# Kernel optimization log

Measured on AMD Instinct MI355X. Metric: run time of the kernel, lower is better.

## Reference

```python
import jax, jax.numpy as jnp
import numpy as np

B, C_IN, T = 8, 1024, 8192
K, D = 1024, 8  # codebook_size, codebook_dim


def setup_inputs() -> dict:
    key = jax.random.key(0)
    ks = jax.random.split(key, 6)
    z = jax.random.normal(ks[0], (B, C_IN, T), dtype=jnp.float32)
    # effective (post weight-norm) 1x1 conv weights, kernel dim squeezed
    in_w = jax.random.normal(ks[1], (D, C_IN), dtype=jnp.float32) * (1.0 / np.sqrt(C_IN))
    in_b = jax.random.normal(ks[2], (D,), dtype=jnp.float32) * 0.01
    codebook = jax.random.normal(ks[3], (K, D), dtype=jnp.float32)
    out_w = jax.random.normal(ks[4], (C_IN, D), dtype=jnp.float32) * (1.0 / np.sqrt(D))
    out_b = jax.random.normal(ks[5], (C_IN,), dtype=jnp.float32) * 0.01
    return {"z": z, "in_w": in_w, "in_b": in_b, "codebook": codebook,
            "out_w": out_w, "out_b": out_b}


def reference(z, in_w, in_b, codebook, out_w, out_b):
    # in_proj: 1x1 Conv1d over channels  [B,C,T] -> [B,D,T]
    z_e = jnp.einsum('bct,dc->bdt', z, in_w) + in_b[None, :, None]
    enc = z_e.transpose(0, 2, 1).reshape(-1, z_e.shape[1])  # [B*T, D]
    # squared-L2 distance to every codebook entry: ||e||^2 - 2 e.w + ||w||^2
    dist = ((enc * enc).sum(1, keepdims=True)
            - 2.0 * enc @ codebook.T
            + (codebook * codebook).sum(1)[None, :])  # [B*T, K]
    ids = jnp.argmax(-dist, axis=1).reshape(z.shape[0], -1)  # [B, T]
    # decode: embedding gather + 1x1 out_proj  [B,T,D] -> [B,C,T]
    z_q = codebook[ids]  # [B, T, D]
    out = jnp.einsum('btd,cd->bct', z_q, out_w) + out_b[None, :, None]
    return out, ids
```

## Files before the change

kernel.cpp:

```cpp
#include <hip/hip_runtime.h>

#define B_   8
#define C_   1024
#define T_   8192
#define K_   1024
#define D_   8
#define CT_  (C_ * T_)
#define BT_  (B_ * T_)
#define OUTN_ ((size_t)B_ * CT_)

__global__ __launch_bounds__(256) void vq_encode_kernel(
    const float* __restrict__ z, const float* __restrict__ in_w,
    const float* __restrict__ in_b, const float* __restrict__ cb,
    float* __restrict__ ids_f)
{
    __shared__ float s_inwT[C_ * D_];
    __shared__ float s_nrm[K_];
    __shared__ float s_encp[4][D_][64];
    __shared__ float s_val[4][64];
    __shared__ int   s_idx[4][64];

    const int tid = threadIdx.x;
    const int w   = tid >> 6;
    const int l   = tid & 63;
    const int bt0 = blockIdx.x * 64;
    const int b   = bt0 >> 13;
    const int t0  = bt0 & (T_ - 1);

    for (int i = tid; i < C_ * D_; i += 256) {
        const int d = i >> 10;
        const int c = i & (C_ - 1);
        s_inwT[c * D_ + d] = in_w[i];
    }
    {
        float ib[D_];
#pragma unroll
        for (int d = 0; d < D_; ++d) ib[d] = in_b[d];
#pragma unroll
        for (int j = 0; j < 4; ++j) {
            const int k = tid + j * 256;
            const float4* cp = (const float4*)(cb + k * D_);
            const float4 a = cp[0], q = cp[1];
            const float ss = a.x*a.x + a.y*a.y + a.z*a.z + a.w*a.w
                           + q.x*q.x + q.y*q.y + q.z*q.z + q.w*q.w;
            const float qq = ib[0]*a.x + ib[1]*a.y + ib[2]*a.z + ib[3]*a.w
                           + ib[4]*q.x + ib[5]*q.y + ib[6]*q.z + ib[7]*q.w;
            s_nrm[k] = 0.5f * ss - qq;
        }
    }
    __syncthreads();

    float acc[D_];
#pragma unroll
    for (int d = 0; d < D_; ++d) acc[d] = 0.0f;
    const float* zp = z + (size_t)b * CT_ + (size_t)(w * 256) * T_ + (t0 + l);
#pragma unroll 8
    for (int i = 0; i < 256; ++i) {
        const float zv = zp[(size_t)i * T_];
        const float4* wp = (const float4*)&s_inwT[(w * 256 + i) * D_];
        const float4 w0 = wp[0], w1 = wp[1];
        acc[0] = fmaf(zv, w0.x, acc[0]);
        acc[1] = fmaf(zv, w0.y, acc[1]);
        acc[2] = fmaf(zv, w0.z, acc[2]);
        acc[3] = fmaf(zv, w0.w, acc[3]);
        acc[4] = fmaf(zv, w1.x, acc[4]);
        acc[5] = fmaf(zv, w1.y, acc[5]);
        acc[6] = fmaf(zv, w1.z, acc[6]);
        acc[7] = fmaf(zv, w1.w, acc[7]);
    }
#pragma unroll
    for (int d = 0; d < D_; ++d) s_encp[w][d][l] = acc[d];
    __syncthreads();

    for (int p = tid; p < 512; p += 256) {
        const int d = p >> 6, tt = p & 63;
        s_encp[0][d][tt] = s_encp[0][d][tt] + s_encp[1][d][tt]
                         + s_encp[2][d][tt] + s_encp[3][d][tt];
    }
    __syncthreads();

    float e[D_];
#pragma unroll
    for (int d = 0; d < D_; ++d) e[d] = s_encp[0][d][l];

    const int wu = __builtin_amdgcn_readfirstlane(w);
    float best = 3.4e38f;
    int   bi   = 0;
    for (int j = 0; j < 256; ++j) {
        const int k = wu * 256 + j;
        const float4* cp = (const float4*)(cb + k * D_);
        const float4 a = cp[0], q = cp[1];
        float s = s_nrm[k];
        s = fmaf(-e[0], a.x, s);
        s = fmaf(-e[1], a.y, s);
        s = fmaf(-e[2], a.z, s);
        s = fmaf(-e[3], a.w, s);
        s = fmaf(-e[4], q.x, s);
        s = fmaf(-e[5], q.y, s);
        s = fmaf(-e[6], q.z, s);
        s = fmaf(-e[7], q.w, s);
        if (s < best) { best = s; bi = k; }
    }
    s_val[w][l] = best;
    s_idx[w][l] = bi;
    __syncthreads();

    if (tid < 64) {
        float bv = s_val[0][l];
        int   bb = s_idx[0][l];
#pragma unroll
        for (int ww = 1; ww < 4; ++ww) {
            const float v = s_val[ww][l];
            if (v < bv) { bv = v; bb = s_idx[ww][l]; }
        }
        ids_f[bt0 + l] = (float)bb;
    }
}

__global__ __launch_bounds__(256) void vq_decode_kernel(
    const float* __restrict__ ids_f, const float* __restrict__ cb,
    const float* __restrict__ out_w, const float* __restrict__ out_b,
    float* __restrict__ out)
{
    __shared__ float s_cbT[D_ * K_];

    const int tid = threadIdx.x;
    for (int i = tid; i < K_ * D_ / 4; i += 256) {
        const float4 v = ((const float4*)cb)[i];
        const int k = i >> 1;
        const int d0 = (i & 1) * 4;
        s_cbT[(d0 + 0) * K_ + k] = v.x;
        s_cbT[(d0 + 1) * K_ + k] = v.y;
        s_cbT[(d0 + 2) * K_ + k] = v.z;
        s_cbT[(d0 + 3) * K_ + k] = v.w;
    }
    __syncthreads();

    const int blk = blockIdx.x;
    const int bt0 = (blk >> 3) * 1024;
    const int c0  = (blk & 7) * 128;
    const int b   = bt0 >> 13;
    const int tt  = (bt0 & (T_ - 1)) + tid * 4;

    const float4 idv = *(const float4*)(ids_f + bt0 + tid * 4);
    const int k0 = (int)idv.x, k1 = (int)idv.y, k2 = (int)idv.z, k3 = (int)idv.w;

    float r0[D_], r1[D_], r2[D_], r3[D_];
#pragma unroll
    for (int d = 0; d < D_; ++d) {
        r0[d] = s_cbT[d * K_ + k0];
        r1[d] = s_cbT[d * K_ + k1];
        r2[d] = s_cbT[d * K_ + k2];
        r3[d] = s_cbT[d * K_ + k3];
    }

    float* op = out + (size_t)b * CT_ + (size_t)c0 * T_ + tt;
#pragma unroll 4
    for (int j = 0; j < 128; ++j) {
        const int c = c0 + j;
        const float4* wp = (const float4*)(out_w + c * D_);
        const float4 w0 = wp[0], w1 = wp[1];
        const float bias = out_b[c];
        float wr[D_];
        wr[0] = w0.x; wr[1] = w0.y; wr[2] = w0.z; wr[3] = w0.w;
        wr[4] = w1.x; wr[5] = w1.y; wr[6] = w1.z; wr[7] = w1.w;
        float4 o;
        o.x = bias; o.y = bias; o.z = bias; o.w = bias;
#pragma unroll
        for (int d = 0; d < D_; ++d) {
            o.x = fmaf(r0[d], wr[d], o.x);
            o.y = fmaf(r1[d], wr[d], o.y);
            o.z = fmaf(r2[d], wr[d], o.z);
            o.w = fmaf(r3[d], wr[d], o.w);
        }
        *(float4*)(op + (size_t)j * T_) = o;
    }
}

extern "C" void kernel_launch(void* const* d_in, const int* in_sizes, int n_in,
                              void* d_out, int out_size, void* d_ws, size_t ws_size,
                              hipStream_t stream) {
    const float* z    = (const float*)d_in[0];
    const float* in_w = (const float*)d_in[1];
    const float* in_b = (const float*)d_in[2];
    const float* cb   = (const float*)d_in[3];
    const float* ow   = (const float*)d_in[4];
    const float* ob   = (const float*)d_in[5];

    float* out   = (float*)d_out;
    float* ids_f = out + OUTN_;

    vq_encode_kernel<<<BT_ / 64, 256, 0, stream>>>(z, in_w, in_b, cb, ids_f);
    vq_decode_kernel<<<(BT_ / 1024) * 8, 256, 0, stream>>>(ids_f, cb, ow, ob, out);
}
```

Measured before the change: 554.7 us.

## Fuse encode and decode into one kernel with a separate prep kernel

Moves the transposed in_proj weights and the codebook norm/bias term into a small prep kernel that writes to workspace, so the main kernel no longer fills 36KB of LDS per block. Encode, argmin and decode now run in one kernel: each block decodes its own 64 timesteps using the chosen codebook rows staged in LDS, which removes the ids round trip and the second launch. The smaller LDS footprint and launch_bounds(256,4) are meant to raise occupancy. In exchange, weights are read from global/scalar memory instead of LDS, and output stores become scalar 64-wide rows instead of float4.

```diff
diff --git a/kernel.cpp b/kernel.cpp
--- a/kernel.cpp
+++ b/kernel.cpp
@@ -9,171 +9,117 @@
 #define BT_  (B_ * T_)
 #define OUTN_ ((size_t)B_ * CT_)
 
-__global__ __launch_bounds__(256) void vq_encode_kernel(
-    const float* __restrict__ z, const float* __restrict__ in_w,
-    const float* __restrict__ in_b, const float* __restrict__ cb,
-    float* __restrict__ ids_f)
+__global__ __launch_bounds__(256) void vq_prep(
+    const float* __restrict__ in_w, const float* __restrict__ in_b,
+    const float* __restrict__ cb, float* __restrict__ wT,
+    float* __restrict__ nrm)
 {
-    __shared__ float s_inwT[C_ * D_];
-    __shared__ float s_nrm[K_];
-    __shared__ float s_encp[4][D_][64];
-    __shared__ float s_val[4][64];
-    __shared__ int   s_idx[4][64];
+    const int i = blockIdx.x * 256 + threadIdx.x;
+    if (i < C_ * D_) {
+        const int d = i >> 10;
+        const int c = i & (C_ - 1);
+        wT[c * D_ + d] = in_w[i];
+    }
+    if (i < K_) {
+        float s = 0.0f, q = 0.0f;
+#pragma unroll
+        for (int d = 0; d < D_; ++d) {
+            const float w = cb[i * D_ + d];
+            s = fmaf(w, w, s);
+            q = fmaf(in_b[d], w, q);
+        }
+        nrm[i] = 0.5f * s - q;
+    }
+}
+
+__global__ __launch_bounds__(256, 4) void vq_fused(
+    const float* __restrict__ z, const float* __restrict__ wT,
+    const float* __restrict__ nrm, const float* __restrict__ cb,
+    const float* __restrict__ out_w, const float* __restrict__ out_b,
+    float* __restrict__ out, float* __restrict__ ids_f)
+{
+    __shared__ float s_p[2048];
 
     const int tid = threadIdx.x;
-    const int w   = tid >> 6;
+    const int wu  = __builtin_amdgcn_readfirstlane(tid >> 6);
     const int l   = tid & 63;
     const int bt0 = blockIdx.x * 64;
     const int b   = bt0 >> 13;
     const int t0  = bt0 & (T_ - 1);
-
-    for (int i = tid; i < C_ * D_; i += 256) {
-        const int d = i >> 10;
-        const int c = i & (C_ - 1);
-        s_inwT[c * D_ + d] = in_w[i];
-    }
-    {
-        float ib[D_];
-#pragma unroll
-        for (int d = 0; d < D_; ++d) ib[d] = in_b[d];
-#pragma unroll
-        for (int j = 0; j < 4; ++j) {
-            const int k = tid + j * 256;
-            const float4* cp = (const float4*)(cb + k * D_);
-            const float4 a = cp[0], q = cp[1];
-            const float ss = a.x*a.x + a.y*a.y + a.z*a.z + a.w*a.w
-                           + q.x*q.x + q.y*q.y + q.z*q.z + q.w*q.w;
-            const float qq = ib[0]*a.x + ib[1]*a.y + ib[2]*a.z + ib[3]*a.w
-                           + ib[4]*q.x + ib[5]*q.y + ib[6]*q.z + ib[7]*q.w;
-            s_nrm[k] = 0.5f * ss - qq;
-        }
-    }
-    __syncthreads();
+    const int c0  = wu * 256;
 
     float acc[D_];
 #pragma unroll
     for (int d = 0; d < D_; ++d) acc[d] = 0.0f;
-    const float* zp = z + (size_t)b * CT_ + (size_t)(w * 256) * T_ + (t0 + l);
-#pragma unroll 8
-    for (int i = 0; i < 256; ++i) {
-        const float zv = zp[(size_t)i * T_];
-        const float4* wp = (const float4*)&s_inwT[(w * 256 + i) * D_];
-        const float4 w0 = wp[0], w1 = wp[1];
-        acc[0] = fmaf(zv, w0.x, acc[0]);
-        acc[1] = fmaf(zv, w0.y, acc[1]);
-        acc[2] = fmaf(zv, w0.z, acc[2]);
-        acc[3] = fmaf(zv, w0.w, acc[3]);
-        acc[4] = fmaf(zv, w1.x, acc[4]);
-        acc[5] = fmaf(zv, w1.y, acc[5]);
-        acc[6] = fmaf(zv, w1.z, acc[6]);
-        acc[7] = fmaf(zv, w1.w, acc[7]);
+
+    const float* zp = z + (size_t)b * CT_ + (size_t)c0 * T_ + (t0 + l);
+    for (int i0 = 0; i0 < 256; i0 += 16) {
+        float zv[16];
+#pragma unroll
+        for (int u = 0; u < 16; ++u) zv[u] = zp[(size_t)(i0 + u) * T_];
+#pragma unroll
+        for (int u = 0; u < 16; ++u) {
+            const float* wr = wT + (size_t)(c0 + i0 + u) * D_;
+#pragma unroll
+            for (int d = 0; d < D_; ++d) acc[d] = fmaf(zv[u], wr[d], acc[d]);
+        }
     }
 #pragma unroll
-    for (int d = 0; d < D_; ++d) s_encp[w][d][l] = acc[d];
+    for (int d = 0; d < D_; ++d) s_p[wu * 512 + d * 64 + l] = acc[d];
     __syncthreads();
 
-    for (int p = tid; p < 512; p += 256) {
-        const int d = p >> 6, tt = p & 63;
-        s_encp[0][d][tt] = s_encp[0][d][tt] + s_encp[1][d][tt]
-                         + s_encp[2][d][tt] + s_encp[3][d][tt];
-    }
+    for (int p = tid; p < 512; p += 256)
+        s_p[p] = s_p[p] + s_p[512 + p] + s_p[1024 + p] + s_p[1536 + p];
     __syncthreads();
 
     float e[D_];
 #pragma unroll
-    for (int d = 0; d < D_; ++d) e[d] = s_encp[0][d][l];
+    for (int d = 0; d < D_; ++d) e[d] = s_p[d * 64 + l];
 
-    const int wu = __builtin_amdgcn_readfirstlane(w);
     float best = 3.4e38f;
     int   bi   = 0;
     for (int j = 0; j < 256; ++j) {
-        const int k = wu * 256 + j;
-        const float4* cp = (const float4*)(cb + k * D_);
-        const float4 a = cp[0], q = cp[1];
-        float s = s_nrm[k];
-        s = fmaf(-e[0], a.x, s);
-        s = fmaf(-e[1], a.y, s);
-        s = fmaf(-e[2], a.z, s);
-        s = fmaf(-e[3], a.w, s);
-        s = fmaf(-e[4], q.x, s);
-        s = fmaf(-e[5], q.y, s);
-        s = fmaf(-e[6], q.z, s);
-        s = fmaf(-e[7], q.w, s);
+        const int k = c0 + j;
+        const float* cr = cb + (size_t)k * D_;
+        float s = nrm[k];
+#pragma unroll
+        for (int d = 0; d < D_; ++d) s = fmaf(-e[d], cr[d], s);
         if (s < best) { best = s; bi = k; }
     }
-    s_val[w][l] = best;
-    s_idx[w][l] = bi;
+    s_p[1024 + wu * 64 + l] = best;
+    ((int*)s_p)[1280 + wu * 64 + l] = bi;
     __syncthreads();
 
     if (tid < 64) {
-        float bv = s_val[0][l];
-        int   bb = s_idx[0][l];
+        float bv = s_p[1024 + l];
+        int   bb = ((int*)s_p)[1280 + l];
 #pragma unroll
         for (int ww = 1; ww < 4; ++ww) {
-            const float v = s_val[ww][l];
-            if (v < bv) { bv = v; bb = s_idx[ww][l]; }
+            const float v = s_p[1024 + ww * 64 + l];
+            if (v < bv) { bv = v; bb = ((int*)s_p)[1280 + ww * 64 + l]; }
         }
         ids_f[bt0 + l] = (float)bb;
-    }
-}
-
-__global__ __launch_bounds__(256) void vq_decode_kernel(
-    const float* __restrict__ ids_f, const float* __restrict__ cb,
-    const float* __restrict__ out_w, const float* __restrict__ out_b,
-    float* __restrict__ out)
-{
-    __shared__ float s_cbT[D_ * K_];
-
-    const int tid = threadIdx.x;
-    for (int i = tid; i < K_ * D_ / 4; i += 256) {
-        const float4 v = ((const float4*)cb)[i];
-        const int k = i >> 1;
-        const int d0 = (i & 1) * 4;
-        s_cbT[(d0 + 0) * K_ + k] = v.x;
-        s_cbT[(d0 + 1) * K_ + k] = v.y;
-        s_cbT[(d0 + 2) * K_ + k] = v.z;
-        s_cbT[(d0 + 3) * K_ + k] = v.w;
+        const float4* cp = (const float4*)(cb + (size_t)bb * D_);
+        const float4 a = cp[0], q = cp[1];
+        float* zq = s_p + l * D_;
+        zq[0] = a.x; zq[1] = a.y; zq[2] = a.z; zq[3] = a.w;
+        zq[4] = q.x; zq[5] = q.y; zq[6] = q.z; zq[7] = q.w;
     }
     __syncthreads();
 
-    const int blk = blockIdx.x;
-    const int bt0 = (blk >> 3) * 1024;
-    const int c0  = (blk & 7) * 128;
-    const int b   = bt0 >> 13;
-    const int tt  = (bt0 & (T_ - 1)) + tid * 4;
+    float r[D_];
+#pragma unroll
+    for (int d = 0; d < D_; ++d) r[d] = s_p[l * D_ + d];
 
-    const float4 idv = *(const float4*)(ids_f + bt0 + tid * 4);
-    const int k0 = (int)idv.x, k1 = (int)idv.y, k2 = (int)idv.z, k3 = (int)idv.w;
-
-    float r0[D_], r1[D_], r2[D_], r3[D_];
+    float* op = out + (size_t)b * CT_ + (size_t)c0 * T_ + (t0 + l);
+#pragma unroll 8
+    for (int j = 0; j < 256; ++j) {
+        const int c = c0 + j;
+        const float* wr = out_w + (size_t)c * D_;
+        float o = out_b[c];
 #pragma unroll
-    for (int d = 0; d < D_; ++d) {
-        r0[d] = s_cbT[d * K_ + k0];
-        r1[d] = s_cbT[d * K_ + k1];
-        r2[d] = s_cbT[d * K_ + k2];
-        r3[d] = s_cbT[d * K_ + k3];
-    }
-
-    float* op = out + (size_t)b * CT_ + (size_t)c0 * T_ + tt;
-#pragma unroll 4
-    for (int j = 0; j < 128; ++j) {
-        const int c = c0 + j;
-        const float4* wp = (const float4*)(out_w + c * D_);
-        const float4 w0 = wp[0], w1 = wp[1];
-        const float bias = out_b[c];
-        float wr[D_];
-        wr[0] = w0.x; wr[1] = w0.y; wr[2] = w0.z; wr[3] = w0.w;
-        wr[4] = w1.x; wr[5] = w1.y; wr[6] = w1.z; wr[7] = w1.w;
-        float4 o;
-        o.x = bias; o.y = bias; o.z = bias; o.w = bias;
-#pragma unroll
-        for (int d = 0; d < D_; ++d) {
-            o.x = fmaf(r0[d], wr[d], o.x);
-            o.y = fmaf(r1[d], wr[d], o.y);
-            o.z = fmaf(r2[d], wr[d], o.z);
-            o.w = fmaf(r3[d], wr[d], o.w);
-        }
-        *(float4*)(op + (size_t)j * T_) = o;
+        for (int d = 0; d < D_; ++d) o = fmaf(r[d], wr[d], o);
+        op[(size_t)j * T_] = o;
     }
 }
 
@@ -190,6 +136,9 @@
     float* out   = (float*)d_out;
     float* ids_f = out + OUTN_;
 
-    vq_encode_kernel<<<BT_ / 64, 256, 0, stream>>>(z, in_w, in_b, cb, ids_f);
-    vq_decode_kernel<<<(BT_ / 1024) * 8, 256, 0, stream>>>(ids_f, cb, ow, ob, out);
+    float* wT  = (float*)d_ws;
+    float* nrm = wT + C_ * D_;
+
+    vq_prep<<<32, 256, 0, stream>>>(in_w, in_b, cb, wT, nrm);
+    vq_fused<<<BT_ / 64, 256, 0, stream>>>(z, wT, nrm, cb, ow, ob, out, ids_f);
 }
```

Result: faster. 523.8 us (-5.6%).
